# Optimization experiments

Measured on AMD Instinct MI355X. Metric: run time of the kernel, lower is better.

## Reference

```python
import jax, jax.numpy as jnp
import numpy as np

DIM = 1024
NUM_HEADS = 16
HEAD_DIM = DIM // NUM_HEADS
SCALE = HEAD_DIM ** (-0.5)


def setup_inputs() -> dict:
    key = jax.random.key(0)
    k_x, k_qkv, k_ow, k_ob = jax.random.split(key, 4)
    x = jax.random.normal(k_x, (4, 2048, DIM), dtype=jnp.float32)
    # nn.Linear(dim, 3*dim, bias=False): store as [dim, 3*dim] for x @ W
    w_qkv = jax.random.normal(k_qkv, (DIM, 3 * DIM), dtype=jnp.float32) * (DIM ** -0.5)
    w_out = jax.random.normal(k_ow, (DIM, DIM), dtype=jnp.float32) * (DIM ** -0.5)
    b_out = jax.random.normal(k_ob, (DIM,), dtype=jnp.float32) * 0.02
    return {"x": x, "w_qkv": w_qkv, "w_out": w_out, "b_out": b_out}


def reference(x, w_qkv, w_out, b_out):
    B, S, D = x.shape
    H, Hd = NUM_HEADS, HEAD_DIM
    qkv = x @ w_qkv                                  # [B, S, 3*D]
    # rearrange 'b s (v h d) -> v b h s d'
    qkv = qkv.reshape(B, S, 3, H, Hd).transpose(2, 0, 3, 1, 4)
    q, k, v = qkv[0], qkv[1], qkv[2]                 # each [B, H, S, Hd]
    scores = jnp.einsum('bhqd,bhkd->bhqk', q, k) * SCALE
    attn = jax.nn.softmax(scores, axis=-1)
    out = jnp.einsum('bhqk,bhkd->bhqd', attn, v)     # [B, H, S, Hd]
    out = out.transpose(0, 2, 1, 3).reshape(B, S, D)  # 'b h s d -> b s (h d)'
    return out @ w_out + b_out
```

## Files before the change

### kernel.cpp

```cpp
#include <hip/hip_runtime.h>
#include <hip/hip_bf16.h>
#include <stdint.h>

typedef __bf16 bf16_t;
typedef __bf16 bf16x4 __attribute__((ext_vector_type(4)));
typedef __bf16 bf16x8 __attribute__((ext_vector_type(8)));
typedef float f32x4 __attribute__((ext_vector_type(4)));
typedef unsigned short u16;

#define L2E 1.4426950408889634f
#define MC 69.249473f

__device__ __forceinline__ void async_load16(const bf16_t* g, bf16_t* l) {
  __builtin_amdgcn_global_load_lds(
      (__attribute__((address_space(1))) uint32_t*)g,
      (__attribute__((address_space(3))) uint32_t*)l, 16, 0, 0);
}

__global__ void detect_k(const uint16_t* __restrict__ x, int* __restrict__ flag) {
  if (threadIdx.x == 0 && blockIdx.x == 0) {
    int bad = 0;
    for (int i = 0; i < 256; ++i) {
      uint16_t h = x[2 * i];
      int e = (h >> 7) & 0xFF;
      if (e == 0 || e >= 0xBD) bad++;
    }
    *flag = (bad > 32) ? 1 : 0;
  }
}

__global__ void convert_k(const void* __restrict__ in, bf16_t* __restrict__ out,
                          int n, const int* __restrict__ flag) {
  const int f = *flag;
  const int i0 = blockIdx.x * blockDim.x + threadIdx.x;
  const int stride = gridDim.x * blockDim.x;
  if (f) {
    const float* p = (const float*)in;
    for (int i = i0; i < n; i += stride) {
      float v = p[i];
      v = (v == v) ? v : 0.f;
      v = fminf(fmaxf(v, -1e6f), 1e6f);
      out[i] = (bf16_t)v;
    }
  } else {
    const bf16_t* p = (const bf16_t*)in;
    for (int i = i0; i < n; i += stride) {
      float v = (float)p[i];
      v = (v == v) ? v : 0.f;
      v = fminf(fmaxf(v, -1e6f), 1e6f);
      out[i] = (bf16_t)v;
    }
  }
}

__global__ __launch_bounds__(256) void wtrans_k(const void* __restrict__ in,
                                                bf16_t* __restrict__ out, int R,
                                                int C, const int* __restrict__ flag) {
  __shared__ u16 tile[64][65];
  const int f = *flag;
  const int tr = blockIdx.y * 64, tc = blockIdx.x * 64;
  const int t = threadIdx.x;
#pragma unroll
  for (int i = 0; i < 16; ++i) {
    int idx = i * 256 + t, r = idx >> 6, c = idx & 63;
    float v;
    if (f)
      v = ((const float*)in)[(size_t)(tr + r) * C + tc + c];
    else
      v = (float)((const bf16_t*)in)[(size_t)(tr + r) * C + tc + c];
    v = (v == v) ? v : 0.f;
    v = fminf(fmaxf(v, -1e6f), 1e6f);
    bf16_t b = (bf16_t)v;
    tile[r][c] = *(u16*)&b;
  }
  __syncthreads();
#pragma unroll
  for (int i = 0; i < 16; ++i) {
    int idx = i * 256 + t, r = idx >> 6, c = idx & 63;
    ((u16*)out)[(size_t)(tc + r) * R + tr + c] = tile[c][r];
  }
}

__device__ __forceinline__ void gemm_bt_mainloop(
    const bf16_t* __restrict__ A, const bf16_t* __restrict__ Bt, int K, int m0,
    int n0, bf16_t* As, bf16_t* Bs, f32x4 acc[4][4]) {
  const int t = threadIdx.x, lane = t & 63, w = t >> 6;
  const int l15 = lane & 15, quad = lane >> 4;
  const int wm = (w >> 1) * 64, wn = (w & 1) * 64;
  const int srow = w * 16 + (lane >> 2);
  const int sk = (lane & 3) * 8;
  const bf16_t* gA = A + (size_t)(m0 + srow) * K + sk;
  const bf16_t* gB = Bt + (size_t)(n0 + srow) * K + sk;
  bf16_t* lA = As + w * 512;
  bf16_t* lB = Bs + w * 512;
  const size_t gstep = (size_t)64 * K;

  for (int kt = 0; kt < K; kt += 32) {
    __syncthreads();
    async_load16(gA, lA);
    async_load16(gA + gstep, lA + 2048);
    async_load16(gB, lB);
    async_load16(gB + gstep, lB + 2048);
    gA += 32;
    gB += 32;
    __syncthreads();
    bf16x8 af[4], bfr[4];
#pragma unroll
    for (int f = 0; f < 4; ++f) {
      af[f] = *(const bf16x8*)(As + (wm + f * 16 + l15) * 32 + quad * 8);
      bfr[f] = *(const bf16x8*)(Bs + (wn + f * 16 + l15) * 32 + quad * 8);
    }
#pragma unroll
    for (int i = 0; i < 4; ++i)
#pragma unroll
      for (int j = 0; j < 4; ++j)
        acc[i][j] =
            __builtin_amdgcn_mfma_f32_16x16x32_bf16(af[i], bfr[j], acc[i][j], 0, 0, 0);
  }
}

__global__ __launch_bounds__(256) void qkv_gemm_k(const bf16_t* __restrict__ X,
                                                  const bf16_t* __restrict__ WqT,
                                                  bf16_t* __restrict__ qo,
                                                  bf16_t* __restrict__ ko,
                                                  bf16_t* __restrict__ vo) {
  __shared__ __align__(16) bf16_t As[128 * 32];
  __shared__ __align__(16) bf16_t Bs[128 * 32];
  const int m0 = blockIdx.y * 128, n0 = blockIdx.x * 128;
  f32x4 acc[4][4];
  const f32x4 z = {0.f, 0.f, 0.f, 0.f};
#pragma unroll
  for (int i = 0; i < 4; ++i)
#pragma unroll
    for (int j = 0; j < 4; ++j) acc[i][j] = z;
  gemm_bt_mainloop(X, WqT, 1024, m0, n0, As, Bs, acc);

  const int lane = threadIdx.x & 63, w = threadIdx.x >> 6;
  const int l15 = lane & 15, quad = lane >> 4;
  const int wm = (w >> 1) * 64, wn = (w & 1) * 64;
#pragma unroll
  for (int j = 0; j < 4; ++j) {
    const int gnb = n0 + wn + j * 16;
    const int vi = gnb >> 10;
    const int rem = gnb & 1023;
    const int h = rem >> 6;
    const int d = (rem & 63) + l15;
    const float scale = (vi == 0) ? 0.125f : 1.0f;
    bf16_t* dst = (vi == 0) ? qo : ((vi == 1) ? ko : vo);
#pragma unroll
    for (int i = 0; i < 4; ++i) {
#pragma unroll
      for (int r = 0; r < 4; ++r) {
        const int gm = m0 + wm + i * 16 + quad * 4 + r;
        const int b = gm >> 11, s = gm & 2047;
        dst[(((size_t)(b * 16 + h) * 2048 + s) << 6) + d] =
            (bf16_t)(acc[i][j][r] * scale);
      }
    }
  }
}

__global__ __launch_bounds__(256) void vtrans_k(const u16* __restrict__ in,
                                                u16* __restrict__ out) {
  __shared__ u16 tile[64][65];
  const int bh = blockIdx.y, st = blockIdx.x;
  const u16* src = in + ((size_t)bh * 2048 + st * 64) * 64;
  u16* dst = out + (size_t)bh * 64 * 2048 + st * 64;
  const int t = threadIdx.x;
#pragma unroll
  for (int i = 0; i < 16; ++i) {
    int idx = i * 256 + t, r = idx >> 6, c = idx & 63;
    tile[r][c] = src[(size_t)r * 64 + c];
  }
  __syncthreads();
#pragma unroll
  for (int i = 0; i < 16; ++i) {
    int idx = i * 256 + t, r = idx >> 6, c = idx & 63;
    dst[(size_t)r * 2048 + c] = tile[c][r];
  }
}

__global__ __launch_bounds__(256) void out_gemm_k(const bf16_t* __restrict__ Ain,
                                                  const bf16_t* __restrict__ WoT,
                                                  const bf16_t* __restrict__ bias,
                                                  void* __restrict__ outp,
                                                  const int* __restrict__ flag) {
  __shared__ __align__(16) bf16_t As[128 * 32];
  __shared__ __align__(16) bf16_t Bs[128 * 32];
  const int m0 = blockIdx.y * 128, n0 = blockIdx.x * 128;
  f32x4 acc[4][4];
  const f32x4 z = {0.f, 0.f, 0.f, 0.f};
#pragma unroll
  for (int i = 0; i < 4; ++i)
#pragma unroll
    for (int j = 0; j < 4; ++j) acc[i][j] = z;
  gemm_bt_mainloop(Ain, WoT, 1024, m0, n0, As, Bs, acc);

  const int f32out = *flag;
  const int lane = threadIdx.x & 63, w = threadIdx.x >> 6;
  const int l15 = lane & 15, quad = lane >> 4;
  const int wm = (w >> 1) * 64, wn = (w & 1) * 64;
#pragma unroll
  for (int j = 0; j < 4; ++j) {
    const int gn = n0 + wn + j * 16 + l15;
    const float bv = (float)bias[gn];
#pragma unroll
    for (int i = 0; i < 4; ++i) {
#pragma unroll
      for (int r = 0; r < 4; ++r) {
        const int gm = m0 + wm + i * 16 + quad * 4 + r;
        const float val = acc[i][j][r] + bv;
        if (f32out)
          ((float*)outp)[(size_t)gm * 1024 + gn] = val;
        else
          ((bf16_t*)outp)[(size_t)gm * 1024 + gn] = (bf16_t)val;
      }
    }
  }
}

#define AST 72
#define KTILE 4096

__global__ __launch_bounds__(256) void attn_k(const bf16_t* __restrict__ q,
                                              const bf16_t* __restrict__ k,
                                              const bf16_t* __restrict__ vt,
                                              bf16_t* __restrict__ o) {
  __shared__ __align__(16) bf16_t QPs[128 * AST];
  __shared__ __align__(16) bf16_t Ks[2 * KTILE];
  __shared__ __align__(16) bf16_t Vts[2 * KTILE];

  const int t = threadIdx.x, lane = t & 63, w = t >> 6;
  const int l15 = lane & 15, quad = lane >> 4;
  const int x = blockIdx.x;
  const int j = x >> 3;
  const int bh = (x & 7) * 8 + (j >> 4);
  const int qt = j & 15;
  const bf16_t* qp = q + ((size_t)bh * 2048 + qt * 128) * 64;
  const bf16_t* kp = k + (size_t)bh * 2048 * 64;
  const bf16_t* vp = vt + (size_t)bh * 64 * 2048;

  const int lane8 = lane >> 3, lc = lane & 7;
  int kOff[2], vOff[2], ldsOff[2];
#pragma unroll
  for (int c = 0; c < 2; ++c) {
    const int rho = (w * 2 + c) * 8 + lane8;
    const int srow = (rho >> 4) + (rho & 15) * 4;
    const int col = (lc ^ (rho & 7)) * 8;
    kOff[c] = srow * 64 + col;
    vOff[c] = rho * 2048 + col;
    ldsOff[c] = (w * 2 + c) * 512;
  }

#pragma unroll
  for (int c = 0; c < 2; ++c) {
    async_load16(kp + kOff[c], Ks + ldsOff[c]);
    async_load16(vp + vOff[c], Vts + ldsOff[c]);
  }

#pragma unroll
  for (int p = 0; p < 4; ++p) {
    const int idx = p * 256 + t, r = idx >> 3, c8 = (idx & 7) * 8;
    *(uint4*)(QPs + r * AST + c8) = *(const uint4*)(qp + (size_t)r * 64 + c8);
  }
  __syncthreads();

  bf16x8 qf[2][2];
#pragma unroll
  for (int qs = 0; qs < 2; ++qs)
#pragma unroll
    for (int ks = 0; ks < 2; ++ks)
      qf[qs][ks] = *(const bf16x8*)(QPs + (w * 32 + qs * 16 + l15) * AST +
                                    ks * 32 + quad * 8);

  f32x4 acc[2][4];
  const f32x4 z = {0.f, 0.f, 0.f, 0.f};
  float lsum[2][4];
#pragma unroll
  for (int qs = 0; qs < 2; ++qs)
#pragma unroll
    for (int f = 0; f < 4; ++f) {
      acc[qs][f] = z;
      lsum[qs][f] = 0.f;
    }

  bf16_t* psw = QPs + w * 32 * AST;

  for (int kt = 0; kt < 32; ++kt) {
    const int b = kt & 1;
    if (kt < 31) {
      const int bn = b ^ 1;
#pragma unroll
      for (int c = 0; c < 2; ++c) {
        async_load16(kp + (size_t)(kt + 1) * KTILE + kOff[c],
                     Ks + bn * KTILE + ldsOff[c]);
        async_load16(vp + (size_t)(kt + 1) * 64 + vOff[c],
                     Vts + bn * KTILE + ldsOff[c]);
      }
    }

    const bf16_t* Kb = Ks + b * KTILE;
    const bf16_t* Vb = Vts + b * KTILE;

    f32x4 sacc[2][4];
#pragma unroll
    for (int qs = 0; qs < 2; ++qs)
#pragma unroll
      for (int f = 0; f < 4; ++f) sacc[qs][f] = z;
#pragma unroll
    for (int ks = 0; ks < 2; ++ks) {
      const int cx = (((ks * 4 + quad) ^ (l15 & 7)) * 8);
      bf16x8 kf[4];
#pragma unroll
      for (int f = 0; f < 4; ++f)
        kf[f] = *(const bf16x8*)(Kb + (f * 16 + l15) * 64 + cx);
      __builtin_amdgcn_s_setprio(1);
#pragma unroll
      for (int qs = 0; qs < 2; ++qs)
#pragma unroll
        for (int f = 0; f < 4; ++f)
          sacc[qs][f] = __builtin_amdgcn_mfma_f32_16x16x32_bf16(
              qf[qs][ks], kf[f], sacc[qs][f], 0, 0, 0);
      __builtin_amdgcn_s_setprio(0);
    }

#pragma unroll
    for (int qs = 0; qs < 2; ++qs)
#pragma unroll
      for (int r = 0; r < 4; ++r) {
        bf16x4 pk;
        float ls = 0.f;
#pragma unroll
        for (int f = 0; f < 4; ++f) {
          const float pv = __builtin_amdgcn_exp2f(
              fminf(fmaf(sacc[qs][f][r], L2E, -MC), 0.f));
          ls += pv;
          pk[f] = (bf16_t)pv;
        }
        lsum[qs][r] += ls;
        *(bf16x4*)(psw + (qs * 16 + quad * 4 + r) * AST + 4 * l15) = pk;
      }

#pragma unroll
    for (int ks = 0; ks < 2; ++ks) {
      const int cx = (((ks * 4 + quad) ^ (l15 & 7)) * 8);
      bf16x8 vf[4];
#pragma unroll
      for (int f = 0; f < 4; ++f)
        vf[f] = *(const bf16x8*)(Vb + (f * 16 + l15) * 64 + cx);
      __builtin_amdgcn_s_setprio(1);
#pragma unroll
      for (int qs = 0; qs < 2; ++qs) {
        bf16x8 pf =
            *(const bf16x8*)(psw + (qs * 16 + l15) * AST + ks * 32 + quad * 8);
#pragma unroll
        for (int f = 0; f < 4; ++f)
          acc[qs][f] = __builtin_amdgcn_mfma_f32_16x16x32_bf16(
              pf, vf[f], acc[qs][f], 0, 0, 0);
      }
      __builtin_amdgcn_s_setprio(0);
    }

    if (kt < 31) __syncthreads();
  }

#pragma unroll
  for (int qs = 0; qs < 2; ++qs)
#pragma unroll
    for (int r = 0; r < 4; ++r) {
      float s = lsum[qs][r];
      s += __shfl_xor(s, 1, 64);
      s += __shfl_xor(s, 2, 64);
      s += __shfl_xor(s, 4, 64);
      s += __shfl_xor(s, 8, 64);
      lsum[qs][r] = 1.0f / fmaxf(s, 1e-37f);
    }

  const int b = bh >> 4, h = bh & 15;
#pragma unroll
  for (int qs = 0; qs < 2; ++qs)
#pragma unroll
    for (int r = 0; r < 4; ++r) {
      const int srow = qt * 128 + w * 32 + qs * 16 + quad * 4 + r;
      const float inv = lsum[qs][r];
#pragma unroll
      for (int f = 0; f < 4; ++f) {
        const int d = f * 16 + l15;
        o[(size_t)(b * 2048 + srow) * 1024 + h * 64 + d] =
            (bf16_t)(acc[qs][f][r] * inv);
      }
    }
}

extern "C" void kernel_launch(void* const* d_in, const int* in_sizes, int n_in,
                              void* d_out, int out_size, void* d_ws, size_t ws_size,
                              hipStream_t stream) {
  const void* x_raw = d_in[0];
  const void* wqkv_raw = d_in[1];
  const void* wout_raw = d_in[2];
  const void* bout_raw = d_in[3];

  const int nx = 4 * 2048 * 1024;
  const int nwq = 1024 * 3072;
  const int nwo = 1024 * 1024;
  const int nb = 1024;

  char* ws = (char*)d_ws;
  int* flag = (int*)ws;
  bf16_t* xb = (bf16_t*)(ws + 256);
  bf16_t* wqbT = xb + nx;
  bf16_t* wobT = wqbT + nwq;
  bf16_t* bob = wobT + nwo;
  bf16_t* qb = bob + nb;
  const size_t bhsd = (size_t)4 * 16 * 2048 * 64;
  bf16_t* kb = qb + bhsd;
  bf16_t* vb = kb + bhsd;
  bf16_t* vtb = xb;
  bf16_t* ab = vb;

  detect_k<<<1, 64, 0, stream>>>((const uint16_t*)x_raw, flag);
  convert_k<<<2048, 256, 0, stream>>>(x_raw, xb, nx, flag);
  wtrans_k<<<dim3(3072 / 64, 1024 / 64), 256, 0, stream>>>(wqkv_raw, wqbT, 1024,
                                                           3072, flag);
  wtrans_k<<<dim3(1024 / 64, 1024 / 64), 256, 0, stream>>>(wout_raw, wobT, 1024,
                                                           1024, flag);
  convert_k<<<4, 256, 0, stream>>>(bout_raw, bob, nb, flag);

  qkv_gemm_k<<<dim3(3072 / 128, 8192 / 128), 256, 0, stream>>>(xb, wqbT, qb, kb, vb);
  vtrans_k<<<dim3(32, 64), 256, 0, stream>>>((const u16*)vb, (u16*)vtb);
  attn_k<<<dim3(1024), 256, 0, stream>>>(qb, kb, vtb, ab);
  out_gemm_k<<<dim3(1024 / 128, 8192 / 128), 256, 0, stream>>>(ab, wobT, bob,
                                                               d_out, flag);
}
```

Baseline: 336.2 us.

## Halve attention query tile to 64 rows and double grid size

```diff
diff --git a/kernel.cpp b/kernel.cpp
--- a/kernel.cpp
+++ b/kernel.cpp
@@ -219,14 +219,13 @@
   }
 }
 
-#define AST 72
 #define KTILE 4096
 
 __global__ __launch_bounds__(256) void attn_k(const bf16_t* __restrict__ q,
                                               const bf16_t* __restrict__ k,
                                               const bf16_t* __restrict__ vt,
                                               bf16_t* __restrict__ o) {
-  __shared__ __align__(16) bf16_t QPs[128 * AST];
+  __shared__ __align__(16) bf16_t Ps[64 * 64];
   __shared__ __align__(16) bf16_t Ks[2 * KTILE];
   __shared__ __align__(16) bf16_t Vts[2 * KTILE];
 
@@ -234,9 +233,9 @@
   const int l15 = lane & 15, quad = lane >> 4;
   const int x = blockIdx.x;
   const int j = x >> 3;
-  const int bh = (x & 7) * 8 + (j >> 4);
-  const int qt = j & 15;
-  const bf16_t* qp = q + ((size_t)bh * 2048 + qt * 128) * 64;
+  const int bh = (x & 7) * 8 + (j >> 5);
+  const int qt = j & 31;
+  const bf16_t* qp = q + ((size_t)bh * 2048 + qt * 64) * 64;
   const bf16_t* kp = k + (size_t)bh * 2048 * 64;
   const bf16_t* vp = vt + (size_t)bh * 64 * 2048;
 
@@ -257,34 +256,28 @@
     async_load16(kp + kOff[c], Ks + ldsOff[c]);
     async_load16(vp + vOff[c], Vts + ldsOff[c]);
   }
-
-#pragma unroll
-  for (int p = 0; p < 4; ++p) {
-    const int idx = p * 256 + t, r = idx >> 3, c8 = (idx & 7) * 8;
-    *(uint4*)(QPs + r * AST + c8) = *(const uint4*)(qp + (size_t)r * 64 + c8);
+#pragma unroll
+  for (int p = 0; p < 2; ++p) {
+    const int off = p * 2048 + w * 512 + lane * 8;
+    async_load16(qp + off, Ps + off);
   }
   __syncthreads();
 
-  bf16x8 qf[2][2];
-#pragma unroll
-  for (int qs = 0; qs < 2; ++qs)
-#pragma unroll
-    for (int ks = 0; ks < 2; ++ks)
-      qf[qs][ks] = *(const bf16x8*)(QPs + (w * 32 + qs * 16 + l15) * AST +
-                                    ks * 32 + quad * 8);
-
-  f32x4 acc[2][4];
+  bf16x8 qf[2];
+#pragma unroll
+  for (int ks = 0; ks < 2; ++ks)
+    qf[ks] = *(const bf16x8*)(Ps + (w * 16 + l15) * 64 + ks * 32 + quad * 8);
+
+  f32x4 acc[4];
   const f32x4 z = {0.f, 0.f, 0.f, 0.f};
-  float lsum[2][4];
-#pragma unroll
-  for (int qs = 0; qs < 2; ++qs)
-#pragma unroll
-    for (int f = 0; f < 4; ++f) {
-      acc[qs][f] = z;
-      lsum[qs][f] = 0.f;
-    }
-
-  bf16_t* psw = QPs + w * 32 * AST;
+  float lsum[4];
+#pragma unroll
+  for (int f = 0; f < 4; ++f) {
+    acc[f] = z;
+    lsum[f] = 0.f;
+  }
+
+  bf16_t* psw = Ps + w * 1024;
 
   for (int kt = 0; kt < 32; ++kt) {
     const int b = kt & 1;
@@ -302,11 +295,9 @@
     const bf16_t* Kb = Ks + b * KTILE;
     const bf16_t* Vb = Vts + b * KTILE;
 
-    f32x4 sacc[2][4];
-#pragma unroll
-    for (int qs = 0; qs < 2; ++qs)
-#pragma unroll
-      for (int f = 0; f < 4; ++f) sacc[qs][f] = z;
+    f32x4 sacc[4];
+#pragma unroll
+    for (int f = 0; f < 4; ++f) sacc[f] = z;
 #pragma unroll
     for (int ks = 0; ks < 2; ++ks) {
       const int cx = (((ks * 4 + quad) ^ (l15 & 7)) * 8);
@@ -316,30 +307,28 @@
         kf[f] = *(const bf16x8*)(Kb + (f * 16 + l15) * 64 + cx);
       __builtin_amdgcn_s_setprio(1);
 #pragma unroll
-      for (int qs = 0; qs < 2; ++qs)
-#pragma unroll
-        for (int f = 0; f < 4; ++f)
-          sacc[qs][f] = __builtin_amdgcn_mfma_f32_16x16x32_bf16(
-              qf[qs][ks], kf[f], sacc[qs][f], 0, 0, 0);
+      for (int f = 0; f < 4; ++f)
+        sacc[f] = __builtin_amdgcn_mfma_f32_16x16x32_bf16(qf[ks], kf[f],
+                                                          sacc[f], 0, 0, 0);
       __builtin_amdgcn_s_setprio(0);
     }
 
 #pragma unroll
-    for (int qs = 0; qs < 2; ++qs)
-#pragma unroll
-      for (int r = 0; r < 4; ++r) {
-        bf16x4 pk;
-        float ls = 0.f;
-#pragma unroll
-        for (int f = 0; f < 4; ++f) {
-          const float pv = __builtin_amdgcn_exp2f(
-              fminf(fmaf(sacc[qs][f][r], L2E, -MC), 0.f));
-          ls += pv;
-          pk[f] = (bf16_t)pv;
-        }
-        lsum[qs][r] += ls;
-        *(bf16x4*)(psw + (qs * 16 + quad * 4 + r) * AST + 4 * l15) = pk;
+    for (int r = 0; r < 4; ++r) {
+      bf16x4 pk;
+      float ls = 0.f;
+#pragma unroll
+      for (int f = 0; f < 4; ++f) {
+        const float pv =
+            __builtin_amdgcn_exp2f(fminf(fmaf(sacc[f][r], L2E, -MC), 0.f));
+        ls += pv;
+        pk[f] = (bf16_t)pv;
       }
+      lsum[r] += ls;
+      const int row = quad * 4 + r;
+      *(bf16x4*)(psw + row * 64 + ((l15 >> 1) ^ (row & 7)) * 8 +
+                 (l15 & 1) * 4) = pk;
+    }
 
 #pragma unroll
     for (int ks = 0; ks < 2; ++ks) {
@@ -348,16 +337,13 @@
 #pragma unroll
       for (int f = 0; f < 4; ++f)
         vf[f] = *(const bf16x8*)(Vb + (f * 16 + l15) * 64 + cx);
+      bf16x8 pf = *(const bf16x8*)(psw + l15 * 64 +
+                                   ((ks * 4 + quad) ^ (l15 & 7)) * 8);
       __builtin_amdgcn_s_setprio(1);
 #pragma unroll
-      for (int qs = 0; qs < 2; ++qs) {
-        bf16x8 pf =
-            *(const bf16x8*)(psw + (qs * 16 + l15) * AST + ks * 32 + quad * 8);
-#pragma unroll
-        for (int f = 0; f < 4; ++f)
-          acc[qs][f] = __builtin_amdgcn_mfma_f32_16x16x32_bf16(
-              pf, vf[f], acc[qs][f], 0, 0, 0);
-      }
+      for (int f = 0; f < 4; ++f)
+        acc[f] = __builtin_amdgcn_mfma_f32_16x16x32_bf16(pf, vf[f], acc[f], 0,
+                                                         0, 0);
       __builtin_amdgcn_s_setprio(0);
     }
 
@@ -365,31 +351,27 @@
   }
 
 #pragma unroll
-  for (int qs = 0; qs < 2; ++qs)
-#pragma unroll
-    for (int r = 0; r < 4; ++r) {
-      float s = lsum[qs][r];
-      s += __shfl_xor(s, 1, 64);
-      s += __shfl_xor(s, 2, 64);
-      s += __shfl_xor(s, 4, 64);
-      s += __shfl_xor(s, 8, 64);
-      lsum[qs][r] = 1.0f / fmaxf(s, 1e-37f);
-    }
+  for (int r = 0; r < 4; ++r) {
+    float s = lsum[r];
+    s += __shfl_xor(s, 1, 64);
+    s += __shfl_xor(s, 2, 64);
+    s += __shfl_xor(s, 4, 64);
+    s += __shfl_xor(s, 8, 64);
+    lsum[r] = 1.0f / fmaxf(s, 1e-37f);
+  }
 
   const int b = bh >> 4, h = bh & 15;
 #pragma unroll
-  for (int qs = 0; qs < 2; ++qs)
-#pragma unroll
-    for (int r = 0; r < 4; ++r) {
-      const int srow = qt * 128 + w * 32 + qs * 16 + quad * 4 + r;
-      const float inv = lsum[qs][r];
-#pragma unroll
-      for (int f = 0; f < 4; ++f) {
-        const int d = f * 16 + l15;
-        o[(size_t)(b * 2048 + srow) * 1024 + h * 64 + d] =
-            (bf16_t)(acc[qs][f][r] * inv);
-      }
-    }
+  for (int r = 0; r < 4; ++r) {
+    const int srow = qt * 64 + w * 16 + quad * 4 + r;
+    const float inv = lsum[r];
+#pragma unroll
+    for (int f = 0; f < 4; ++f) {
+      const int d = f * 16 + l15;
+      o[(size_t)(b * 2048 + srow) * 1024 + h * 64 + d] =
+          (bf16_t)(acc[f][r] * inv);
+    }
+  }
 }
 
 extern "C" void kernel_launch(void* const* d_in, const int* in_sizes, int n_in,
@@ -428,7 +410,7 @@
 
   qkv_gemm_k<<<dim3(3072 / 128, 8192 / 128), 256, 0, stream>>>(xb, wqbT, qb, kb, vb);
   vtrans_k<<<dim3(32, 64), 256, 0, stream>>>((const u16*)vb, (u16*)vtb);
-  attn_k<<<dim3(1024), 256, 0, stream>>>(qb, kb, vtb, ab);
+  attn_k<<<dim3(2048), 256, 0, stream>>>(qb, kb, vtb, ab);
   out_gemm_k<<<dim3(1024 / 128, 8192 / 128), 256, 0, stream>>>(ab, wobT, bob,
                                                                d_out, flag);
 }
```

Measured after the change: 337.0 us. About the same (+0.3%).
